# Optimization experiments

Measured on AMD Instinct MI355X. Metric: run time of the kernel, lower is better.

The kernel has to match this reference:

```python
import jax, jax.numpy as jnp
import numpy as np

B, N, D = 8, 2048, 768


def setup_inputs() -> dict:
    key = jax.random.key(0)
    ks = jax.random.split(key, 12)
    s = 1.0 / np.sqrt(D)
    inp = {
        "query": jax.random.normal(ks[0], (B, N, D), dtype=jnp.float32),
        "value": jax.random.normal(ks[1], (B, N, D), dtype=jnp.float32),
        "mask": jax.random.randint(ks[2], (B, N), 0, 2, dtype=jnp.int32),
        "q_w": jax.random.uniform(ks[3], (D, D), jnp.float32, -s, s),
        "q_b": jax.random.uniform(ks[4], (D,), jnp.float32, -s, s),
        "k_w": jax.random.uniform(ks[5], (D, D), jnp.float32, -s, s),
        "k_b": jax.random.uniform(ks[6], (D,), jnp.float32, -s, s),
        "v_w": jax.random.uniform(ks[7], (D, D), jnp.float32, -s, s),
        "v_b": jax.random.uniform(ks[8], (D,), jnp.float32, -s, s),
        "fc_w": jax.random.uniform(ks[9], (D, D), jnp.float32, -s, s),
        "fc_b": jax.random.uniform(ks[10], (D,), jnp.float32, -s, s),
    }
    # guarantee at least one unmasked key per batch to avoid all--inf softmax rows
    inp["mask"] = inp["mask"].at[:, 0].set(1)
    return inp


def reference(query, value, mask, q_w, q_b, k_w, k_b, v_w, v_b, fc_w, fc_b):
    # torch Linear: y = x @ W.T + b  (dim==768 branch of the module)
    q = jnp.einsum("bnd,ed->bne", query, q_w) + q_b   # [B,N,D]
    k = jnp.einsum("bnd,ed->bne", value, k_w) + k_b   # [B,N,D]
    v = jnp.einsum("bnd,ed->bne", value, v_w) + v_b   # [B,N,D]
    # unscaled scores, as in the original (no 1/sqrt(d))
    scores = jnp.einsum("bqd,bkd->bqk", q, k)         # [B,N,N]
    key_mask = mask[:, None, :] != 0                  # [B,1,N]
    scores = jnp.where(key_mask, scores, -jnp.inf)
    attn = jax.nn.softmax(scores, axis=2)
    merged = jnp.einsum("bqk,bkd->bqd", attn, v)      # [B,N,D]
    merged = merged * mask[:, :, None].astype(merged.dtype)
    return jnp.einsum("bnd,ed->bne", merged, fc_w) + fc_b
```

## Files before the change

kernel.cpp:

```cpp
#include <hip/hip_runtime.h>
#include <hip/hip_bf16.h>

using bf16 = __hip_bfloat16;
typedef __attribute__((ext_vector_type(4))) float f32x4;
typedef __attribute__((ext_vector_type(8))) __bf16 bf16x8;
typedef __attribute__((ext_vector_type(4))) unsigned int u32x4;
typedef unsigned short u16;

#define LOG2E 1.4426950408889634f
#define SHIFT2 69.24936192747498f

__device__ __forceinline__ void gload_lds16(const void* g, void* l) {
  __builtin_amdgcn_global_load_lds((const __attribute__((address_space(1))) void*)g,
                                   (__attribute__((address_space(3))) void*)l, 16, 0, 0);
}

__device__ __forceinline__ bf16x8 lds_frag(const bf16* p) {
  u32x4 u = *(const u32x4*)p;
  return __builtin_bit_cast(bf16x8, u);
}

__device__ __forceinline__ u16 bf_bits(float v) {
  return __builtin_bit_cast(u16, __float2bfloat16(v));
}

struct GArgs {
  const bf16* Ah; const bf16* Al; long lda; long strideA;
  const bf16* Bh; const bf16* Bl; long ldb; long strideB;
  void* Ch; void* Cl; long ldc; long strideC;
  int K;
  const float* bias;
  float* rowsum; long rsStride;
  const int* idx; const int* cnt;
};

template<bool SPLIT, int CMODE, bool BIAS, bool RSCALE, bool CSCAT, bool SQUARE, bool RAGK>
__global__ __launch_bounds__(256, 2) void gemm_nt(GArgs ga)
{
  const int tid = threadIdx.x;
  const int lane15 = tid & 15;
  const int quad = (tid >> 4) & 3;
  const int wave = tid >> 6;
  const int wm = (wave >> 1) * 64;
  const int wn = (wave & 1) * 64;

  constexpr int KW = SPLIT ? 64 : 32;
  __shared__ alignas(16) bf16 As[128 * KW];
  __shared__ alignas(16) bf16 Bs[128 * KW];
  __shared__ float rowacc[128];
  __shared__ int sT[8];
  __shared__ int sTz[8];

  if (tid < 8) {
    const int Tm = (ga.cnt[tid] + 127) >> 7;
    sT[tid] = Tm;
    sTz[tid] = SQUARE ? Tm * Tm : Tm * 6;
  }
  __syncthreads();
  int total = 0;
  #pragma unroll
  for (int i = 0; i < 8; ++i) total += sTz[i];

  for (int t = blockIdx.x; t < total; t += gridDim.x) {
    int z = 0, rem = t;
    while (rem >= sTz[z]) { rem -= sTz[z]; ++z; }
    const int Tm = sT[z];
    int mt, nt;
    if constexpr (SQUARE) { mt = rem / Tm; nt = rem - mt * Tm; }
    else                  { mt = rem / 6;  nt = rem - mt * 6; }
    const long m0 = (long)mt * 128;
    const long n0 = (long)nt * 128;
    const int cnt = ga.cnt[z];
    const int K = RAGK ? Tm * 128 : ga.K;

    const bf16* Bbh = ga.Bh + z * ga.strideB;
    const bf16* Bbl = SPLIT ? (ga.Bl + z * ga.strideB) : nullptr;
    const bf16* Abh = ga.Ah + (long)z * ga.strideA;
    const bf16* Abl = SPLIT ? (ga.Al + (long)z * ga.strideA) : nullptr;

    f32x4 acc[4][4];
    #pragma unroll
    for (int i = 0; i < 4; ++i)
      #pragma unroll
      for (int j = 0; j < 4; ++j) acc[i][j] = (f32x4){0.f, 0.f, 0.f, 0.f};

    for (int k0 = 0; k0 < K; k0 += 32) {
      __syncthreads();
      if constexpr (SPLIT) {
        #pragma unroll
        for (int r = 0; r < 4; ++r) {
          const int idx = r * 256 + tid, row = idx >> 3, slot = idx & 7;
          const int flip = row & 1, sw = (row >> 1) & 3;
          const int h = (slot >> 2) ^ flip, s = (slot & 3) ^ sw;
          gload_lds16((h ? Bbl : Bbh) + (n0 + row) * ga.ldb + k0 + s * 8, &Bs[idx * 8]);
          gload_lds16((h ? Abl : Abh) + (m0 + row) * ga.lda + k0 + s * 8, &As[idx * 8]);
        }
      } else {
        #pragma unroll
        for (int r = 0; r < 2; ++r) {
          const int idx = r * 256 + tid, row = idx >> 2, slot = idx & 3;
          const int sw = (row >> 1) & 3;
          gload_lds16(Bbh + (n0 + row) * ga.ldb + k0 + (slot ^ sw) * 8, &Bs[idx * 8]);
          gload_lds16(Abh + (m0 + row) * ga.lda + k0 + (slot ^ sw) * 8, &As[idx * 8]);
        }
      }
      __syncthreads();

      const int swl = (lane15 >> 1) & 3;
      if constexpr (SPLIT) {
        const int eff = ((lane15 & 1) << 2) | (quad ^ swl);
        bf16x8 ah[4], al[4], bh[4], bl[4];
        #pragma unroll
        for (int tt = 0; tt < 4; ++tt) {
          const int ar = (wm + tt * 16 + lane15) * 64;
          const int br = (wn + tt * 16 + lane15) * 64;
          ah[tt] = lds_frag(&As[ar + eff * 8]);
          al[tt] = lds_frag(&As[ar + (eff ^ 4) * 8]);
          bh[tt] = lds_frag(&Bs[br + eff * 8]);
          bl[tt] = lds_frag(&Bs[br + (eff ^ 4) * 8]);
        }
        #pragma unroll
        for (int i = 0; i < 4; ++i)
          #pragma unroll
          for (int j = 0; j < 4; ++j) {
            acc[i][j] = __builtin_amdgcn_mfma_f32_16x16x32_bf16(ah[i], bh[j], acc[i][j], 0, 0, 0);
            acc[i][j] = __builtin_amdgcn_mfma_f32_16x16x32_bf16(al[i], bh[j], acc[i][j], 0, 0, 0);
            acc[i][j] = __builtin_amdgcn_mfma_f32_16x16x32_bf16(ah[i], bl[j], acc[i][j], 0, 0, 0);
          }
      } else {
        const int eff = quad ^ swl;
        bf16x8 ah[4], bh[4];
        #pragma unroll
        for (int tt = 0; tt < 4; ++tt) ah[tt] = lds_frag(&As[(wm + tt * 16 + lane15) * 32 + eff * 8]);
        #pragma unroll
        for (int tt = 0; tt < 4; ++tt) bh[tt] = lds_frag(&Bs[(wn + tt * 16 + lane15) * 32 + eff * 8]);
        #pragma unroll
        for (int i = 0; i < 4; ++i)
          #pragma unroll
          for (int j = 0; j < 4; ++j)
            acc[i][j] = __builtin_amdgcn_mfma_f32_16x16x32_bf16(ah[i], bh[j], acc[i][j], 0, 0, 0);
      }
    }

    const long crow0 = m0 + wm + quad * 4;
    const long ccol0 = n0 + wn + lane15;

    if constexpr (CMODE == 3) {
      bf16* P = (bf16*)ga.Ch + (long)z * ga.strideC;
      __syncthreads();
      if (tid < 128) rowacc[tid] = 0.f;
      __syncthreads();
      bool keep[4];
      #pragma unroll
      for (int tn = 0; tn < 4; ++tn) keep[tn] = (ccol0 + tn * 16) < cnt;
      #pragma unroll
      for (int tm = 0; tm < 4; ++tm) {
        #pragma unroll
        for (int r = 0; r < 4; ++r) {
          const long row = crow0 + tm * 16 + r;
          float rsum = 0.f;
          #pragma unroll
          for (int tn = 0; tn < 4; ++tn) {
            float p = keep[tn] ? exp2f(fmaf(acc[tm][tn][r], LOG2E, -SHIFT2)) : 0.f;
            bf16 pb = __float2bfloat16(p);
            P[row * ga.ldc + ccol0 + tn * 16] = pb;
            rsum += __bfloat162float(pb);
          }
          #pragma unroll
          for (int o = 1; o < 16; o <<= 1) rsum += __shfl_xor(rsum, o, 64);
          if (lane15 == 0) atomicAdd(&rowacc[(int)(row - m0)], rsum);
        }
      }
      __syncthreads();
      if (tid < 128) atomicAdd(&ga.rowsum[z * ga.rsStride + m0 + tid], rowacc[tid]);
      continue;
    }

    float bv[4] = {0.f, 0.f, 0.f, 0.f};
    if constexpr (BIAS) {
      #pragma unroll
      for (int tn = 0; tn < 4; ++tn) bv[tn] = ga.bias[ccol0 + tn * 16];
    }
    if constexpr (CMODE == 2) {
      float* C = (float*)ga.Ch + (long)z * ga.strideC;
      #pragma unroll
      for (int tm = 0; tm < 4; ++tm) {
        #pragma unroll
        for (int r = 0; r < 4; ++r) {
          const long row = crow0 + tm * 16 + r;
          long orow = row;
          bool doStore = true;
          if constexpr (CSCAT) {
            doStore = row < cnt;
            orow = doStore ? (long)ga.idx[(long)z * 2048 + row] : 0;
          }
          if (doStore) {
            #pragma unroll
            for (int tn = 0; tn < 4; ++tn)
              C[orow * ga.ldc + ccol0 + tn * 16] = acc[tm][tn][r] + bv[tn];
          }
        }
      }
    } else if constexpr (CMODE == 1) {
      bf16* Ch = (bf16*)ga.Ch + (long)z * ga.strideC;
      bf16* Cl = (bf16*)ga.Cl + (long)z * ga.strideC;
      #pragma unroll
      for (int tm = 0; tm < 4; ++tm) {
        const long row = crow0 + tm * 16;
        #pragma unroll
        for (int tn = 0; tn < 4; ++tn) {
          const long col = ccol0 + tn * 16;
          #pragma unroll
          for (int r = 0; r < 4; ++r) {
            float val = acc[tm][tn][r] + bv[tn];
            bf16 h = __float2bfloat16(val);
            Ch[(row + r) * ga.ldc + col] = h;
            Cl[(row + r) * ga.ldc + col] = __float2bfloat16(val - __bfloat162float(h));
          }
        }
      }
    } else {
      bf16* Ch = (bf16*)ga.Ch + (long)z * ga.strideC;
      #pragma unroll
      for (int tm = 0; tm < 4; ++tm) {
        const long row = crow0 + tm * 16;
        float rm[4];
        #pragma unroll
        for (int r = 0; r < 4; ++r) {
          float f = 1.f;
          if constexpr (RSCALE) f = 1.0f / ga.rowsum[z * ga.rsStride + row + r];
          rm[r] = f;
        }
        #pragma unroll
        for (int tn = 0; tn < 4; ++tn) {
          const long col = ccol0 + tn * 16;
          #pragma unroll
          for (int r = 0; r < 4; ++r)
            Ch[(row + r) * ga.ldc + col] = __float2bfloat16((acc[tm][tn][r] + bv[tn]) * rm[r]);
        }
      }
    }
  }
}

__global__ __launch_bounds__(256) void compact_kernel(
    const int* __restrict__ mask, int* __restrict__ idx, int* __restrict__ cnt)
{
  const int z = blockIdx.x, tid = threadIdx.x;
  const int* m = mask + (long)z * 2048;
  int* id = idx + (long)z * 2048;
  int v[8]; int c = 0;
  #pragma unroll
  for (int j = 0; j < 8; ++j) { v[j] = m[tid * 8 + j]; c += (v[j] != 0) ? 1 : 0; }
  __shared__ int sc[256];
  sc[tid] = c;
  __syncthreads();
  for (int off = 1; off < 256; off <<= 1) {
    int y = 0;
    if (tid >= off) y = sc[tid - off];
    __syncthreads();
    if (tid >= off) sc[tid] += y;
    __syncthreads();
  }
  int k = sc[tid] - c;
  #pragma unroll
  for (int j = 0; j < 8; ++j)
    if (v[j]) id[k++] = tid * 8 + j;
  __syncthreads();
  const int tot = sc[255];
  if (tid == 0) cnt[z] = tot;
  const int last = id[tot - 1];
  for (int i = tot + tid; i < 2048; i += 256) id[i] = last;
}

__global__ __launch_bounds__(256) void gcvt_kernel(
    const float* __restrict__ query, const float* __restrict__ value,
    const int* __restrict__ idx, const int* __restrict__ cnt,
    bf16* __restrict__ Xqh, bf16* __restrict__ Xql,
    bf16* __restrict__ Xvh, bf16* __restrict__ Xvl)
{
  const int z = blockIdx.y;
  const long r0 = (long)blockIdx.x * 128;
  const int kb = (cnt[z] + 127) & ~127;
  if (r0 >= kb) return;
  const float* src = (blockIdx.z ? value : query) + (long)z * 2048 * 768;
  bf16* oh = (blockIdx.z ? Xvh : Xqh) + ((long)z * 2048 + r0) * 768;
  bf16* ol = (blockIdx.z ? Xvl : Xql) + ((long)z * 2048 + r0) * 768;
  const int* id = idx + (long)z * 2048 + r0;
  for (int i = threadIdx.x; i < 128 * 96; i += 256) {
    const int r = i / 96, c = (i - (i / 96) * 96) * 8;
    const float* s = src + (long)id[r] * 768 + c;
    float tv[8];
    *(f32x4*)tv       = *(const f32x4*)s;
    *(f32x4*)(tv + 4) = *(const f32x4*)(s + 4);
    u32x4 H, L;
    u16* ph = (u16*)&H; u16* pl = (u16*)&L;
    #pragma unroll
    for (int j = 0; j < 8; ++j) {
      bf16 hb = __float2bfloat16(tv[j]);
      ph[j] = __builtin_bit_cast(u16, hb);
      pl[j] = bf_bits(tv[j] - __bfloat162float(hb));
    }
    *(u32x4*)(oh + (long)r * 768 + c) = H;
    *(u32x4*)(ol + (long)r * 768 + c) = L;
  }
}

__global__ __launch_bounds__(256) void cvt4_kernel(
    const float* __restrict__ qw, const float* __restrict__ kw,
    const float* __restrict__ vw, const float* __restrict__ fw,
    bf16* __restrict__ Wqh, bf16* __restrict__ Wql,
    bf16* __restrict__ Wkh, bf16* __restrict__ Wkl,
    bf16* __restrict__ Wvh, bf16* __restrict__ Wfh, int n8)
{
  const int i = blockIdx.x * 256 + threadIdx.x;
  if (i >= n8) return;
  const float* in; bf16* oh; bf16* ol = nullptr;
  switch (blockIdx.y) {
    case 0:  in = qw; oh = Wqh; ol = Wql; break;
    case 1:  in = kw; oh = Wkh; ol = Wkl; break;
    case 2:  in = vw; oh = Wvh; break;
    default: in = fw; oh = Wfh; break;
  }
  float tv[8];
  *(f32x4*)tv       = ((const f32x4*)in)[2 * i];
  *(f32x4*)(tv + 4) = ((const f32x4*)in)[2 * i + 1];
  u32x4 H, L;
  u16* ph = (u16*)&H; u16* pl = (u16*)&L;
  #pragma unroll
  for (int j = 0; j < 8; ++j) {
    bf16 hb = __float2bfloat16(tv[j]);
    ph[j] = __builtin_bit_cast(u16, hb);
    pl[j] = bf_bits(tv[j] - __bfloat162float(hb));
  }
  ((u32x4*)oh)[i] = H;
  if (ol) ((u32x4*)ol)[i] = L;
}

__global__ __launch_bounds__(256) void bias_fill_kernel(
    float* __restrict__ out, const float* __restrict__ fc_b)
{
  const long i = (long)blockIdx.x * 256 + threadIdx.x;
  const int col4 = (int)(i % 192);
  ((f32x4*)out)[i] = *(const f32x4*)(fc_b + col4 * 4);
}

__global__ __launch_bounds__(256) void transpose_kernel(
    const u16* __restrict__ in, u16* __restrict__ out, const int* __restrict__ cnt)
{
  const long z = blockIdx.z;
  const long r0 = (long)blockIdx.x * 64, c0 = (long)blockIdx.y * 64;
  const int kb = (cnt[z] + 127) & ~127;
  if (r0 >= kb) return;
  __shared__ alignas(16) u16 t[64][72];
  const u16* inz = in + z * 2048 * 768;
  u16* outz = out + z * 768 * 2048;
  const int tid = threadIdx.x;
  const int rr = tid >> 3, cs = (tid & 7) * 8;
  #pragma unroll
  for (int i = 0; i < 2; ++i) {
    const int row = rr + i * 32;
    u32x4 v = *(const u32x4*)(inz + (r0 + row) * 768 + c0 + cs);
    *(u32x4*)&t[row][cs] = v;
  }
  __syncthreads();
  #pragma unroll
  for (int i = 0; i < 2; ++i) {
    const int oc = rr + i * 32;
    u32x4 o;
    u16* po = (u16*)&o;
    #pragma unroll
    for (int j = 0; j < 8; ++j) po[j] = t[cs + j][oc];
    *(u32x4*)(outz + (c0 + oc) * 2048 + r0 + cs) = o;
  }
}

extern "C" void kernel_launch(void* const* d_in, const int* in_sizes, int n_in,
                              void* d_out, int out_size, void* d_ws, size_t ws_size,
                              hipStream_t stream) {
  const float* query = (const float*)d_in[0];
  const float* value = (const float*)d_in[1];
  const int*   mask  = (const int*)d_in[2];
  const float* q_w   = (const float*)d_in[3];
  const float* q_b   = (const float*)d_in[4];
  const float* k_w   = (const float*)d_in[5];
  const float* k_b   = (const float*)d_in[6];
  const float* v_w   = (const float*)d_in[7];
  const float* v_b   = (const float*)d_in[8];
  const float* fc_w  = (const float*)d_in[9];
  const float* fc_b  = (const float*)d_in[10];

  const long N = 2048, D = 768;
  const long BD = N * D;
  const int WN = (int)(D * D), W8 = WN / 8;
  const size_t WB = ((size_t)WN * 2 + 255) & ~(size_t)255;
  const size_t XB = ((size_t)8 * BD * 2 + 255) & ~(size_t)255;

  char* wp = (char*)d_ws;
  auto take = [&](size_t bytes) {
    char* p = wp;
    wp += (bytes + 255) & ~(size_t)255;
    return p;
  };
  bf16* Wfh = (bf16*)take(WB);
  char* Pb  = take((size_t)8 * N * N * 2);
  bf16* Wqh = (bf16*)(Pb + 0 * WB);
  bf16* Wql = (bf16*)(Pb + 1 * WB);
  bf16* Wkh = (bf16*)(Pb + 2 * WB);
  bf16* Wkl = (bf16*)(Pb + 3 * WB);
  bf16* Wvh = (bf16*)(Pb + 4 * WB);
  bf16* Xvh = (bf16*)(Pb + 5 * WB);
  bf16* V   = (bf16*)(Pb + 5 * WB + XB);
  bf16* P   = (bf16*)Pb;
  bf16* Xqh = (bf16*)take(XB);
  bf16* Xql = (bf16*)take(XB);
  bf16* Xvl = (bf16*)take(XB);
  bf16* Qh  = (bf16*)take(XB);
  bf16* Ql  = (bf16*)take(XB);
  float* rowsum = (float*)take((size_t)8 * N * sizeof(float));
  int* idx = (int*)take((size_t)8 * N * sizeof(int));
  int* cnt = (int*)take(64);
  bf16* Kh = Xqh;
  bf16* Kl = Xql;
  bf16* VT = Xvl;
  bf16* merged = Qh;

  dim3 blk(256);
  dim3 g512(512);

  compact_kernel<<<dim3(8), blk, 0, stream>>>(mask, idx, cnt);
  gcvt_kernel<<<dim3(16, 8, 2), blk, 0, stream>>>(query, value, idx, cnt,
      Xqh, Xql, Xvh, Xvl);
  cvt4_kernel<<<dim3(288, 4), blk, 0, stream>>>(q_w, k_w, v_w, fc_w,
      Wqh, Wql, Wkh, Wkl, Wvh, Wfh, W8);
  hipMemsetAsync(rowsum, 0, (size_t)8 * N * sizeof(float), stream);
  bias_fill_kernel<<<dim3(12288), blk, 0, stream>>>((float*)d_out, fc_b);

  GArgs a{};
  a.idx = idx; a.cnt = cnt; a.rowsum = rowsum; a.rsStride = N;

  a.Ah = Xqh; a.Al = Xql; a.lda = D; a.strideA = BD;
  a.Bh = Wqh; a.Bl = Wql; a.ldb = D; a.strideB = 0;
  a.Ch = Qh; a.Cl = Ql; a.ldc = D; a.strideC = BD;
  a.K = (int)D; a.bias = q_b;
  gemm_nt<true, 1, true, false, false, false, false><<<g512, blk, 0, stream>>>(a);

  a.Ah = Xvh; a.Al = Xvl;
  a.Bh = Wkh; a.Bl = Wkl;
  a.Ch = Kh; a.Cl = Kl; a.bias = k_b;
  gemm_nt<true, 1, true, false, false, false, false><<<g512, blk, 0, stream>>>(a);

  a.Ah = Xvh; a.Al = nullptr;
  a.Bh = Wvh; a.Bl = nullptr;
  a.Ch = V; a.Cl = nullptr; a.bias = v_b;
  gemm_nt<false, 0, true, false, false, false, false><<<g512, blk, 0, stream>>>(a);

  transpose_kernel<<<dim3(32, 12, 8), blk, 0, stream>>>((const u16*)V, (u16*)VT, cnt);

  a.Ah = Qh; a.Al = Ql; a.lda = D; a.strideA = BD;
  a.Bh = Kh; a.Bl = Kl; a.ldb = D; a.strideB = BD;
  a.Ch = P; a.Cl = nullptr; a.ldc = N; a.strideC = N * N;
  a.K = (int)D; a.bias = nullptr;
  gemm_nt<true, 3, false, false, false, true, false><<<g512, blk, 0, stream>>>(a);

  a.Ah = P; a.Al = nullptr; a.lda = N; a.strideA = N * N;
  a.Bh = VT; a.Bl = nullptr; a.ldb = N; a.strideB = BD;
  a.Ch = merged; a.Cl = nullptr; a.ldc = D; a.strideC = BD;
  gemm_nt<false, 0, false, true, false, false, true><<<g512, blk, 0, stream>>>(a);

  a.Ah = merged; a.lda = D; a.strideA = BD;
  a.Bh = Wfh; a.Bl = nullptr; a.ldb = D; a.strideB = 0;
  a.Ch = d_out; a.Cl = nullptr; a.ldc = D; a.strideC = BD;
  a.K = (int)D; a.bias = fc_b;
  gemm_nt<false, 2, true, false, true, false, false><<<g512, blk, 0, stream>>>(a);
}
```

Measured before the change: 490.3 us.

## Fuse Q and K projections into one launch and raise occupancy to four blocks

Merges the Q and K split-precision projection GEMMs into a single launch that enumerates sixteen virtual batches, selecting the operand set per tile. Launch bounds rise from 2 to 4 blocks per CU and the persistent grid grows from 512 to 1024 blocks, which trades fewer registers per thread for more resident waves. The workspace layout is reorganised: K gets dedicated buffers, P now aliases Xqh, V is placed temporarily in the output buffer, and the bias fill moves after the transpose. The tighter register budget may cause spills, and the buffer aliasing must stay correct.

Result: no change. 497.1 us (+1.4%).

```diff
diff --git a/kernel.cpp b/kernel.cpp
--- a/kernel.cpp
+++ b/kernel.cpp
@@ -32,10 +32,13 @@
   const float* bias;
   float* rowsum; long rsStride;
   const int* idx; const int* cnt;
+  const bf16* Ah2; const bf16* Al2; const bf16* Bh2; const bf16* Bl2;
+  void* Ch2; void* Cl2; const float* bias2;
 };
 
-template<bool SPLIT, int CMODE, bool BIAS, bool RSCALE, bool CSCAT, bool SQUARE, bool RAGK>
-__global__ __launch_bounds__(256, 2) void gemm_nt(GArgs ga)
+template<bool SPLIT, int CMODE, bool BIAS, bool RSCALE, bool CSCAT, bool SQUARE,
+         bool RAGK, bool QK2>
+__global__ __launch_bounds__(256, 4) void gemm_nt(GArgs ga)
 {
   const int tid = threadIdx.x;
   const int lane15 = tid & 15;
@@ -44,26 +47,30 @@
   const int wm = (wave >> 1) * 64;
   const int wn = (wave & 1) * 64;
 
+  constexpr int NZ = QK2 ? 16 : 8;
   constexpr int KW = SPLIT ? 64 : 32;
   __shared__ alignas(16) bf16 As[128 * KW];
   __shared__ alignas(16) bf16 Bs[128 * KW];
   __shared__ float rowacc[128];
   __shared__ int sT[8];
-  __shared__ int sTz[8];
-
-  if (tid < 8) {
-    const int Tm = (ga.cnt[tid] + 127) >> 7;
-    sT[tid] = Tm;
+  __shared__ int sTz[NZ];
+
+  if (tid < 8) sT[tid] = (ga.cnt[tid] + 127) >> 7;
+  __syncthreads();
+  if (tid < NZ) {
+    const int Tm = sT[QK2 ? (tid & 7) : tid];
     sTz[tid] = SQUARE ? Tm * Tm : Tm * 6;
   }
   __syncthreads();
   int total = 0;
   #pragma unroll
-  for (int i = 0; i < 8; ++i) total += sTz[i];
+  for (int i = 0; i < NZ; ++i) total += sTz[i];
 
   for (int t = blockIdx.x; t < total; t += gridDim.x) {
-    int z = 0, rem = t;
-    while (rem >= sTz[z]) { rem -= sTz[z]; ++z; }
+    int vz = 0, rem = t;
+    while (rem >= sTz[vz]) { rem -= sTz[vz]; ++vz; }
+    const int z = QK2 ? (vz & 7) : vz;
+    const int mat = QK2 ? (vz >> 3) : 0;
     const int Tm = sT[z];
     int mt, nt;
     if constexpr (SQUARE) { mt = rem / Tm; nt = rem - mt * Tm; }
@@ -73,10 +80,10 @@
     const int cnt = ga.cnt[z];
     const int K = RAGK ? Tm * 128 : ga.K;
 
-    const bf16* Bbh = ga.Bh + z * ga.strideB;
-    const bf16* Bbl = SPLIT ? (ga.Bl + z * ga.strideB) : nullptr;
-    const bf16* Abh = ga.Ah + (long)z * ga.strideA;
-    const bf16* Abl = SPLIT ? (ga.Al + (long)z * ga.strideA) : nullptr;
+    const bf16* Bbh = ((QK2 && mat) ? ga.Bh2 : ga.Bh) + z * ga.strideB;
+    const bf16* Bbl = SPLIT ? (((QK2 && mat) ? ga.Bl2 : ga.Bl) + z * ga.strideB) : nullptr;
+    const bf16* Abh = ((QK2 && mat) ? ga.Ah2 : ga.Ah) + (long)z * ga.strideA;
+    const bf16* Abl = SPLIT ? (((QK2 && mat) ? ga.Al2 : ga.Al) + (long)z * ga.strideA) : nullptr;
 
     f32x4 acc[4][4];
     #pragma unroll
@@ -176,10 +183,11 @@
       continue;
     }
 
+    const float* bias = (QK2 && mat) ? ga.bias2 : ga.bias;
     float bv[4] = {0.f, 0.f, 0.f, 0.f};
     if constexpr (BIAS) {
       #pragma unroll
-      for (int tn = 0; tn < 4; ++tn) bv[tn] = ga.bias[ccol0 + tn * 16];
+      for (int tn = 0; tn < 4; ++tn) bv[tn] = bias[ccol0 + tn * 16];
     }
     if constexpr (CMODE == 2) {
       float* C = (float*)ga.Ch + (long)z * ga.strideC;
@@ -202,8 +210,8 @@
         }
       }
     } else if constexpr (CMODE == 1) {
-      bf16* Ch = (bf16*)ga.Ch + (long)z * ga.strideC;
-      bf16* Cl = (bf16*)ga.Cl + (long)z * ga.strideC;
+      bf16* Ch = (bf16*)((QK2 && mat) ? ga.Ch2 : ga.Ch) + (long)z * ga.strideC;
+      bf16* Cl = (bf16*)((QK2 && mat) ? ga.Cl2 : ga.Cl) + (long)z * ga.strideC;
       #pragma unroll
       for (int tm = 0; tm < 4; ++tm) {
         const long row = crow0 + tm * 16;
@@ -403,30 +411,29 @@
     return p;
   };
   bf16* Wfh = (bf16*)take(WB);
-  char* Pb  = take((size_t)8 * N * N * 2);
-  bf16* Wqh = (bf16*)(Pb + 0 * WB);
-  bf16* Wql = (bf16*)(Pb + 1 * WB);
-  bf16* Wkh = (bf16*)(Pb + 2 * WB);
-  bf16* Wkl = (bf16*)(Pb + 3 * WB);
-  bf16* Wvh = (bf16*)(Pb + 4 * WB);
-  bf16* Xvh = (bf16*)(Pb + 5 * WB);
-  bf16* V   = (bf16*)(Pb + 5 * WB + XB);
-  bf16* P   = (bf16*)Pb;
+  bf16* Wqh = (bf16*)take(WB);
+  bf16* Wql = (bf16*)take(WB);
+  bf16* Wkh = (bf16*)take(WB);
+  bf16* Wkl = (bf16*)take(WB);
+  bf16* Wvh = (bf16*)take(WB);
   bf16* Xqh = (bf16*)take(XB);
   bf16* Xql = (bf16*)take(XB);
+  bf16* Xvh = (bf16*)take(XB);
   bf16* Xvl = (bf16*)take(XB);
   bf16* Qh  = (bf16*)take(XB);
   bf16* Ql  = (bf16*)take(XB);
+  bf16* Kh  = (bf16*)take(XB);
+  bf16* Kl  = (bf16*)take(XB);
   float* rowsum = (float*)take((size_t)8 * N * sizeof(float));
   int* idx = (int*)take((size_t)8 * N * sizeof(int));
   int* cnt = (int*)take(64);
-  bf16* Kh = Xqh;
-  bf16* Kl = Xql;
+  bf16* P = Xqh;
   bf16* VT = Xvl;
   bf16* merged = Qh;
+  bf16* V = (bf16*)((float*)d_out + (size_t)8 * BD / 2);
 
   dim3 blk(256);
-  dim3 g512(512);
+  dim3 g1024(1024);
 
   compact_kernel<<<dim3(8), blk, 0, stream>>>(mask, idx, cnt);
   gcvt_kernel<<<dim3(16, 8, 2), blk, 0, stream>>>(query, value, idx, cnt,
@@ -434,7 +441,6 @@
   cvt4_kernel<<<dim3(288, 4), blk, 0, stream>>>(q_w, k_w, v_w, fc_w,
       Wqh, Wql, Wkh, Wkl, Wvh, Wfh, W8);
   hipMemsetAsync(rowsum, 0, (size_t)8 * N * sizeof(float), stream);
-  bias_fill_kernel<<<dim3(12288), blk, 0, stream>>>((float*)d_out, fc_b);
 
   GArgs a{};
   a.idx = idx; a.cnt = cnt; a.rowsum = rowsum; a.rsStride = N;
@@ -443,34 +449,38 @@
   a.Bh = Wqh; a.Bl = Wql; a.ldb = D; a.strideB = 0;
   a.Ch = Qh; a.Cl = Ql; a.ldc = D; a.strideC = BD;
   a.K = (int)D; a.bias = q_b;
-  gemm_nt<true, 1, true, false, false, false, false><<<g512, blk, 0, stream>>>(a);
-
-  a.Ah = Xvh; a.Al = Xvl;
-  a.Bh = Wkh; a.Bl = Wkl;
-  a.Ch = Kh; a.Cl = Kl; a.bias = k_b;
-  gemm_nt<true, 1, true, false, false, false, false><<<g512, blk, 0, stream>>>(a);
+  a.Ah2 = Xvh; a.Al2 = Xvl; a.Bh2 = Wkh; a.Bl2 = Wkl;
+  a.Ch2 = Kh; a.Cl2 = Kl; a.bias2 = k_b;
+  gemm_nt<true, 1, true, false, false, false, false, true>
+      <<<g1024, blk, 0, stream>>>(a);
 
   a.Ah = Xvh; a.Al = nullptr;
   a.Bh = Wvh; a.Bl = nullptr;
   a.Ch = V; a.Cl = nullptr; a.bias = v_b;
-  gemm_nt<false, 0, true, false, false, false, false><<<g512, blk, 0, stream>>>(a);
+  gemm_nt<false, 0, true, false, false, false, false, false>
+      <<<g1024, blk, 0, stream>>>(a);
 
   transpose_kernel<<<dim3(32, 12, 8), blk, 0, stream>>>((const u16*)V, (u16*)VT, cnt);
+
+  bias_fill_kernel<<<dim3(12288), blk, 0, stream>>>((float*)d_out, fc_b);
 
   a.Ah = Qh; a.Al = Ql; a.lda = D; a.strideA = BD;
   a.Bh = Kh; a.Bl = Kl; a.ldb = D; a.strideB = BD;
   a.Ch = P; a.Cl = nullptr; a.ldc = N; a.strideC = N * N;
   a.K = (int)D; a.bias = nullptr;
-  gemm_nt<true, 3, false, false, false, true, false><<<g512, blk, 0, stream>>>(a);
+  gemm_nt<true, 3, false, false, false, true, false, false>
+      <<<g1024, blk, 0, stream>>>(a);
 
   a.Ah = P; a.Al = nullptr; a.lda = N; a.strideA = N * N;
   a.Bh = VT; a.Bl = nullptr; a.ldb = N; a.strideB = BD;
   a.Ch = merged; a.Cl = nullptr; a.ldc = D; a.strideC = BD;
-  gemm_nt<false, 0, false, true, false, false, true><<<g512, blk, 0, stream>>>(a);
+  gemm_nt<false, 0, false, true, false, false, true, false>
+      <<<g1024, blk, 0, stream>>>(a);
 
   a.Ah = merged; a.lda = D; a.strideA = BD;
   a.Bh = Wfh; a.Bl = nullptr; a.ldb = D; a.strideB = 0;
   a.Ch = d_out; a.Cl = nullptr; a.ldc = D; a.strideC = BD;
   a.K = (int)D; a.bias = fc_b;
-  gemm_nt<false, 2, true, false, true, false, false><<<g512, blk, 0, stream>>>(a);
-}
+  gemm_nt<false, 2, true, false, true, false, false, false>
+      <<<g1024, blk, 0, stream>>>(a);
+}
```
